# Kernel tuning notes

Hardware: AMD Instinct MI355X
Metric: run time of the kernel (lower is better)

Reference implementation:

```python
import jax, jax.numpy as jnp
import numpy as np

N_USER = 100_000
N_ITEM = 50_000
N = N_USER + N_ITEM           # total nodes
E = 4_800_000                 # nnz of normalized adjacency (avg degree 32)
D = 64                        # embed_size
L = 3                         # number of propagation layers (layer_size=[64,64,64])
B = 4096                      # query batch
EPS = 1e-12                   # F.normalize eps


def setup_inputs() -> dict:
    key = jax.random.key(0)
    ks = jax.random.split(key, 11)
    return {
        "user_emb": jax.random.normal(ks[0], (N_USER, D), jnp.float32) * 0.1,
        "item_emb": jax.random.normal(ks[1], (N_ITEM, D), jnp.float32) * 0.1,
        "W_gc": jax.random.normal(ks[2], (L, D, D), jnp.float32) * 0.1,
        "b_gc": jax.random.normal(ks[3], (L, D), jnp.float32) * 0.01,
        "W_bi": jax.random.normal(ks[4], (L, D, D), jnp.float32) * 0.1,
        "b_bi": jax.random.normal(ks[5], (L, D), jnp.float32) * 0.01,
        # normalized adjacency values ~ 1/deg scale
        "adj_val": jax.random.uniform(ks[6], (E,), jnp.float32) * (1.0 / 32.0),
        "adj_row": jax.random.randint(ks[7], (E,), 0, N, dtype=jnp.int32),
        "adj_col": jax.random.randint(ks[8], (E,), 0, N, dtype=jnp.int32),
        "users": jax.random.randint(ks[9], (B,), 0, N_USER, dtype=jnp.int32),
        "items": jax.random.randint(ks[10], (B,), 0, N_ITEM, dtype=jnp.int32),
    }


def _l2_normalize(x):
    # matches torch.nn.functional.normalize(p=2, dim=1, eps=1e-12)
    n = jnp.sqrt(jnp.sum(x * x, axis=1, keepdims=True))
    return x / jnp.maximum(n, EPS)


def reference(user_emb, item_emb, W_gc, b_gc, W_bi, b_bi,
              adj_val, adj_row, adj_col, users, items):
    ego = jnp.concatenate([user_emb, item_emb], axis=0)   # [N, D]
    all_embeddings = [ego]
    for k in range(L):
        # sparse A_hat @ ego: gather neighbor rows, scale, scatter-add
        msgs = adj_val[:, None] * ego[adj_col]            # [E, D]
        side = jax.ops.segment_sum(msgs, adj_row, num_segments=N)  # [N, D]
        sum_emb = side @ W_gc[k] + b_gc[k]                # GCN branch
        bi_emb = (ego * side) @ W_bi[k] + b_bi[k]         # bi-interaction branch
        ego = jax.nn.leaky_relu(sum_emb + bi_emb, negative_slope=0.2)
        all_embeddings.append(_l2_normalize(ego))
    all_embeddings = jnp.concatenate(all_embeddings, axis=1)  # [N, (L+1)*D]
    u_g = all_embeddings[users]                                # [B, 256]
    i_g = all_embeddings[N_USER + items]                       # [B, 256]
    return u_g, i_g
```

## Files before the change

### kernel.cpp

```cpp
#include <hip/hip_runtime.h>
#include <hip/hip_bf16.h>


#define N_USER 100000
#define N_ITEM 50000
#define N_NODES 150000
#define NE 4800000
#define D 64
#define BROWS 128
#define NBUCK ((N_NODES + BROWS - 1) / BROWS)
#define BCAP 4480
#define NG (N_NODES / 16)
#define NCB 5
#define NBIN (BROWS * NCB)
#define GMW ((N_NODES + 31) / 32)
#define NGL (8192 / 16)

#define SUPSH 12
#define NSUP 37
#define SCAP 133120
#define STG1 (NSUP * SCAP)
#define CH1 4688
#define B1 ((NE + CH1 - 1) / CH1)
#define CPS 27
#define CH2 4931
#define B2 (NSUP * CPS)

typedef __hip_bfloat16 bf16;
typedef unsigned short u16;
typedef unsigned int u32;
typedef __attribute__((ext_vector_type(8))) short short8;
typedef __attribute__((ext_vector_type(4))) float float4v;

__device__ __forceinline__ float bits2f(u16 u) {
  return __uint_as_float(((unsigned int)u) << 16);
}
__device__ __forceinline__ u16 f2bits(float x) {
  union { bf16 h; u16 u; } c;
  c.h = __float2bfloat16(x);
  return c.u;
}
__device__ __forceinline__ float loadF(const void* p, long i, int f32) {
  if (f32) return ((const float*)p)[i];
  return bits2f(((const u16*)p)[i]);
}

__global__ void k_zero(int* __restrict__ p, int n) {
  int i = blockIdx.x * blockDim.x + threadIdx.x;
  if (i < n) p[i] = 0;
}

__global__ void k_detect(const u16* __restrict__ ue, int* __restrict__ flag) {
  int bad = 0;
  for (int t = threadIdx.x; t < 512; t += 256) {
    float f = fabsf(bits2f(ue[t]));
    if (!(f < 1e4f)) bad = 1;
  }
  if (bad) atomicOr(flag, 1);
}

__global__ void __launch_bounds__(1024) k_mark(const int* __restrict__ users,
                                               const int* __restrict__ items,
                                               u32* __restrict__ gmap,
                                               int* __restrict__ rowlist) {
  int tid = threadIdx.x;
  for (int i = tid; i < GMW; i += 1024) gmap[i] = 0;
  __syncthreads();
  for (int b = tid; b < 8192; b += 1024) {
    int r = (b < 4096) ? users[b] : (N_USER + items[b - 4096]);
    rowlist[b] = r;
    atomicOr(&gmap[r >> 5], 1u << (r & 31));
  }
}

__global__ void k_prepw(const void* __restrict__ Wgc, const void* __restrict__ bgc,
                        const void* __restrict__ Wbi, const void* __restrict__ bbi,
                        u16* __restrict__ wfrag, float* __restrict__ biasws,
                        const int* __restrict__ flag) {
  int f32 = *flag;
  int layer = blockIdx.x;
  for (int f = threadIdx.x; f < 8192; f += 512) {
    int j = f & 7;
    int lane = (f >> 3) & 63;
    int s2 = (f >> 9) & 3;
    int t = f >> 11;
    int k = s2 * 32 + (lane >> 4) * 8 + j;
    int n = t * 16 + (lane & 15);
    float w = (k < 64) ? loadF(Wgc, (long)layer * 4096 + k * 64 + n, f32)
                       : loadF(Wbi, (long)layer * 4096 + (k - 64) * 64 + n, f32);
    wfrag[layer * 8192 + f] = f2bits(w);
  }
  if (threadIdx.x < 64)
    biasws[layer * 64 + threadIdx.x] =
        loadF(bgc, layer * 64 + threadIdx.x, f32) +
        loadF(bbi, layer * 64 + threadIdx.x, f32);
}

__global__ void k_init(const void* __restrict__ ue, const void* __restrict__ ie,
                       float* __restrict__ ego32, u16* __restrict__ egobf,
                       const int* __restrict__ flag, const u32* __restrict__ gmap) {
  int f32 = *flag;
  int i4 = (blockIdx.x * blockDim.x + threadIdx.x) * 4;
  if (i4 >= N_NODES * D) return;
  const int UD = N_USER * D;
  float4 v;
  ushort4 b;
  if (f32) {
    const float* s = (i4 < UD) ? ((const float*)ue + i4) : ((const float*)ie + (i4 - UD));
    v = *(const float4*)s;
    b = make_ushort4(f2bits(v.x), f2bits(v.y), f2bits(v.z), f2bits(v.w));
  } else {
    const u16* s = (i4 < UD) ? ((const u16*)ue + i4) : ((const u16*)ie + (i4 - UD));
    b = *(const ushort4*)s;
    v = make_float4(bits2f(b.x), bits2f(b.y), bits2f(b.z), bits2f(b.w));
  }
  int r = i4 >> 6;
  if ((gmap[r >> 5] >> (r & 31)) & 1) *(float4*)(ego32 + i4) = v;
  *(ushort4*)(egobf + i4) = b;
}

__global__ void __launch_bounds__(512, 8) k_bin1(
    const int* __restrict__ row, const int* __restrict__ col,
    const void* __restrict__ val, int* __restrict__ scnt,
    int2* __restrict__ staged1, const int* __restrict__ flag) {
  __shared__ int2 sbuf[CH1];
  __shared__ int hist[NSUP];
  __shared__ int lstart[NSUP];
  __shared__ int gbase[NSUP];
  __shared__ int lcur[NSUP];
  int f32 = *flag;
  int tid = threadIdx.x;
  int e0 = blockIdx.x * CH1;
  int e1 = min(e0 + CH1, NE);
  if (tid < NSUP) hist[tid] = 0;
  __syncthreads();
  for (int e = e0 + tid * 4; e < e1; e += 512 * 4) {
    int4 r4 = *(const int4*)(row + e);
    atomicAdd(&hist[r4.x >> SUPSH], 1);
    atomicAdd(&hist[r4.y >> SUPSH], 1);
    atomicAdd(&hist[r4.z >> SUPSH], 1);
    atomicAdd(&hist[r4.w >> SUPSH], 1);
  }
  __syncthreads();
  int resv = 0;
  if (tid < 64) {
    int h = (tid < NSUP) ? hist[tid] : 0;
    int inc = h;
#pragma unroll
    for (int off = 1; off < 64; off <<= 1) {
      int v = __shfl_up(inc, off);
      if (tid >= off) inc += v;
    }
    if (tid < NSUP) {
      int ex = inc - h;
      lstart[tid] = ex;
      lcur[tid] = ex;
      if (h) resv = atomicAdd(&scnt[tid], h);
    }
  }
  __syncthreads();
  for (int e = e0 + tid * 4; e < e1; e += 512 * 4) {
    int4 r4 = *(const int4*)(row + e);
    int4 c4 = *(const int4*)(col + e);
    int vb[4];
    if (f32) {
      float4 v4 = *(const float4*)((const float*)val + e);
      vb[0] = __float_as_int(v4.x); vb[1] = __float_as_int(v4.y);
      vb[2] = __float_as_int(v4.z); vb[3] = __float_as_int(v4.w);
    } else {
      ushort4 v4 = *(const ushort4*)((const u16*)val + e);
      vb[0] = __float_as_int(bits2f(v4.x)); vb[1] = __float_as_int(bits2f(v4.y));
      vb[2] = __float_as_int(bits2f(v4.z)); vb[3] = __float_as_int(bits2f(v4.w));
    }
    int rr[4] = {r4.x, r4.y, r4.z, r4.w};
    int cc[4] = {c4.x, c4.y, c4.z, c4.w};
#pragma unroll
    for (int j = 0; j < 4; ++j) {
      int s = rr[j] >> SUPSH;
      int pos = atomicAdd(&lcur[s], 1);
      sbuf[pos] = make_int2(((rr[j] & 4095) << 18) | cc[j], vb[j]);
    }
  }
  if (tid < NSUP) gbase[tid] = resv;
  __syncthreads();
  int wv = tid >> 6;
  int ln = tid & 63;
  for (int s = wv; s < NSUP; s += 8) {
    int h = hist[s];
    int gb = gbase[s];
    int ls = lstart[s];
    if (gb + h > SCAP) h = max(0, SCAP - gb);
    int2* dst = staged1 + (size_t)s * SCAP + gb;
    for (int i = ln; i < h; i += 64) dst[i] = sbuf[ls + i];
  }
}

__global__ void __launch_bounds__(512, 8) k_bin2(
    const int* __restrict__ scnt, const int2* __restrict__ staged1,
    int* __restrict__ bcnt, int2* __restrict__ staged2) {
  __shared__ int2 sbuf[CH2];
  __shared__ int hist[32];
  __shared__ int lstart[32];
  __shared__ int gbase[32];
  __shared__ int lcur[32];
  int tid = threadIdx.x;
  int sup = blockIdx.x / CPS;
  int e0 = (blockIdx.x % CPS) * CH2;
  int n = min(scnt[sup], SCAP);
  int e1 = min(e0 + CH2, n);
  if (e0 >= e1) return;
  const int2* seg = staged1 + (size_t)sup * SCAP;
  if (tid < 32) hist[tid] = 0;
  __syncthreads();
  {
    int e = e0 + tid * 2;
    for (; e + 1 < e1; e += 1024) {
      int4 two = *(const int4*)(seg + e);
      atomicAdd(&hist[two.x >> 25], 1);
      atomicAdd(&hist[two.z >> 25], 1);
    }
    if (e < e1) atomicAdd(&hist[seg[e].x >> 25], 1);
  }
  __syncthreads();
  int resv = 0;
  if (tid < 64) {
    int h = (tid < 32) ? hist[tid & 31] : 0;
    int inc = h;
#pragma unroll
    for (int off = 1; off < 32; off <<= 1) {
      int v = __shfl_up(inc, off);
      if (tid >= off) inc += v;
    }
    if (tid < 32) {
      int ex = inc - h;
      lstart[tid] = ex;
      lcur[tid] = ex;
      if (h) resv = atomicAdd(&bcnt[sup * 32 + tid], h);
    }
  }
  __syncthreads();
  {
    int e = e0 + tid * 2;
    for (; e + 1 < e1; e += 1024) {
      int4 two = *(const int4*)(seg + e);
      int lb0 = two.x >> 25;
      int p0 = atomicAdd(&lcur[lb0], 1);
      sbuf[p0] = make_int2(two.x & 0x01FFFFFF, two.y);
      int lb1 = two.z >> 25;
      int p1 = atomicAdd(&lcur[lb1], 1);
      sbuf[p1] = make_int2(two.z & 0x01FFFFFF, two.w);
    }
    if (e < e1) {
      int2 ent = seg[e];
      int lb = ent.x >> 25;
      int pos = atomicAdd(&lcur[lb], 1);
      sbuf[pos] = make_int2(ent.x & 0x01FFFFFF, ent.y);
    }
  }
  if (tid < 32) gbase[tid] = resv;
  __syncthreads();
  int wv = tid >> 6;
  int ln = tid & 63;
  for (int lb = wv; lb < 32; lb += 8) {
    int h = hist[lb];
    int gb = gbase[lb];
    int ls = lstart[lb];
    int b = sup * 32 + lb;
    if (b >= NBUCK) continue;
    if (gb + h > BCAP) h = max(0, BCAP - gb);
    int2* dst = staged2 + (size_t)b * BCAP + gb;
    for (int i = ln; i < h; i += 64) dst[i] = sbuf[ls + i];
  }
}

__global__ void __launch_bounds__(1024) k_bucketbase(const int* __restrict__ bcnt,
                                                     int* __restrict__ bbase) {
  __shared__ int sh[2048];
  int tid = threadIdx.x;
  int t0 = (tid < NBUCK) ? min(bcnt[tid], BCAP) : 0;
  int i1 = 1024 + tid;
  int t1 = (i1 < NBUCK) ? min(bcnt[i1], BCAP) : 0;
  sh[tid] = t0;
  sh[i1] = t1;
  __syncthreads();
  for (int off = 1; off < 2048; off <<= 1) {
    int a0 = (tid >= off) ? sh[tid - off] : 0;
    int a1 = (i1 >= off) ? sh[i1 - off] : 0;
    __syncthreads();
    sh[tid] += a0;
    sh[i1] += a1;
    __syncthreads();
  }
  if (tid < NBUCK) bbase[tid] = sh[tid] - t0;
  if (i1 < NBUCK) bbase[i1] = sh[i1] - t1;
}

__global__ void __launch_bounds__(512, 8) k_sortbucket(
    const int* __restrict__ bcnt, const int2* __restrict__ staged,
    const int* __restrict__ bbase, int* __restrict__ rp, int2* __restrict__ csr) {
  __shared__ int2 sbuf[BCAP];
  __shared__ int hist[NBIN];
  int tid = threadIdx.x;
  int b = blockIdx.x;
  for (int i = tid; i < NBIN; i += 512) hist[i] = 0;
  __syncthreads();

  int n = min(bcnt[b], BCAP);
  const int2* seg = staged + (size_t)b * BCAP;
  {
    int e = tid * 2;
    for (; e + 1 < n; e += 1024) {
      int4 two = *(const int4*)(seg + e);
      atomicAdd(&hist[(two.x >> 18) * NCB + ((two.x >> 15) & 7)], 1);
      atomicAdd(&hist[(two.z >> 18) * NCB + ((two.z >> 15) & 7)], 1);
    }
    if (e < n) {
      int x = seg[e].x;
      atomicAdd(&hist[(x >> 18) * NCB + ((x >> 15) & 7)], 1);
    }
  }
  __syncthreads();

  int i0 = tid, i1 = tid + 512;
  int h0 = hist[i0];
  int h1 = (i1 < NBIN) ? hist[i1] : 0;
  for (int off = 1; off < NBIN; off <<= 1) {
    int v0 = (i0 >= off) ? hist[i0 - off] : 0;
    int v1 = (i1 < NBIN && i1 >= off) ? hist[i1 - off] : 0;
    __syncthreads();
    hist[i0] += v0;
    if (i1 < NBIN) hist[i1] += v1;
    __syncthreads();
  }
  hist[i0] -= h0;
  if (i1 < NBIN) hist[i1] -= h1;
  __syncthreads();

  int base_b = bbase[b];
  if (tid < BROWS) {
    int r = b * BROWS + tid;
    if (r < N_NODES) rp[r] = base_b + hist[tid * NCB];
  }
  if (b == 0 && tid == 0) rp[N_NODES] = NE;
  __syncthreads();

  {
    int e = tid * 2;
    for (; e + 1 < n; e += 1024) {
      int4 two = *(const int4*)(seg + e);
      int k0 = (two.x >> 18) * NCB + ((two.x >> 15) & 7);
      int p0 = atomicAdd(&hist[k0], 1);
      if (p0 < BCAP) sbuf[p0] = make_int2(two.x & 0x3FFFF, two.y);
      int k1 = (two.z >> 18) * NCB + ((two.z >> 15) & 7);
      int p1 = atomicAdd(&hist[k1], 1);
      if (p1 < BCAP) sbuf[p1] = make_int2(two.z & 0x3FFFF, two.w);
    }
    if (e < n) {
      int2 ent = seg[e];
      int k = (ent.x >> 18) * NCB + ((ent.x >> 15) & 7);
      int pos = atomicAdd(&hist[k], 1);
      if (pos < BCAP) sbuf[pos] = make_int2(ent.x & 0x3FFFF, ent.y);
    }
  }
  __syncthreads();

  for (int i = tid; i < n; i += 512) csr[(size_t)base_b + i] = sbuf[i];
}

__global__ void __launch_bounds__(256, 8) k_layer(
    const int* __restrict__ rp, const int2* __restrict__ csr,
    const u16* __restrict__ egobf_i,
    const u16* __restrict__ wfrag, const float* __restrict__ biasws,
    float* __restrict__ ego32_o, u16* __restrict__ egobf_o, int layer,
    const u32* __restrict__ gmap, int last,
    const int* __restrict__ rowlist, int use_list) {
  __shared__ u16 tile[2176];
  int tid = threadIdx.x;
  int lane = tid & 63;
  int ln = lane & 15;
  int quad = lane >> 4;
  int wv = tid >> 6;
  int tg = blockIdx.x;
  const u16* wf = wfrag + layer * 8192;

  {
    int rid = tg * 16 + wv * 4 + quad;
    int r = use_list ? rowlist[rid] : rid;
    int s = rp[r];
    int e = rp[r + 1];
    float4 acc = make_float4(0.f, 0.f, 0.f, 0.f);
    int i = s;
    for (; i + 8 <= e; i += 8) {
      int2 cc[8];
#pragma unroll
      for (int t = 0; t < 8; ++t) cc[t] = csr[i + t];
      ushort4 gg[8];
#pragma unroll
      for (int t = 0; t < 8; ++t)
        gg[t] = *(const ushort4*)(egobf_i + (size_t)cc[t].x * 64 + ln * 4);
#pragma unroll
      for (int t = 0; t < 8; ++t) {
        float v = __int_as_float(cc[t].y);
        acc.x += v * bits2f(gg[t].x);
        acc.y += v * bits2f(gg[t].y);
        acc.z += v * bits2f(gg[t].z);
        acc.w += v * bits2f(gg[t].w);
      }
    }
    for (; i < e; ++i) {
      int2 c = csr[i];
      ushort4 g = *(const ushort4*)(egobf_i + (size_t)c.x * 64 + ln * 4);
      float v = __int_as_float(c.y);
      acc.x += v * bits2f(g.x);
      acc.y += v * bits2f(g.y);
      acc.z += v * bits2f(g.z);
      acc.w += v * bits2f(g.w);
    }
    ushort4 eb = *(const ushort4*)(egobf_i + (size_t)r * 64 + ln * 4);
    float4 er = make_float4(bits2f(eb.x), bits2f(eb.y), bits2f(eb.z), bits2f(eb.w));
    u16* trow = tile + (wv * 4 + quad) * 136;
    *(ushort4*)(trow + ln * 4) =
        make_ushort4(f2bits(acc.x), f2bits(acc.y), f2bits(acc.z), f2bits(acc.w));
    *(ushort4*)(trow + 64 + ln * 4) =
        make_ushort4(f2bits(er.x * acc.x), f2bits(er.y * acc.y),
                     f2bits(er.z * acc.z), f2bits(er.w * acc.w));
  }
  __syncthreads();

  float4v acc2 = (float4v){0.f, 0.f, 0.f, 0.f};
#pragma unroll
  for (int s2 = 0; s2 < 4; ++s2) {
    short8 A = *(const short8*)(tile + (size_t)ln * 136 + s2 * 32 + quad * 8);
    short8 Bf = *(const short8*)(wf + ((size_t)((wv * 4 + s2) * 64 + lane)) * 8);
    acc2 = __builtin_amdgcn_mfma_f32_16x16x32_bf16(A, Bf, acc2, 0, 0, 0);
  }
  int r0 = tg * 16;
  float bt = biasws[layer * 64 + wv * 16 + ln];
#pragma unroll
  for (int g2 = 0; g2 < 4; ++g2) {
    int rid2 = r0 + quad * 4 + g2;
    int rr = use_list ? rowlist[rid2] : rid2;
    float x = acc2[g2] + bt;
    x = fmaxf(x, 0.2f * x);
    size_t idx = (size_t)rr * 64 + wv * 16 + ln;
    if ((gmap[rr >> 5] >> (rr & 31)) & 1) ego32_o[idx] = x;
    if (!last) egobf_o[idx] = f2bits(x);
  }
}

__global__ void k_gather(const float* __restrict__ ego, const int* __restrict__ users,
                         const int* __restrict__ items, void* __restrict__ out,
                         int slice, int do_norm, const int* __restrict__ flag) {
  int f32 = *flag;
  int b = blockIdx.x * 4 + (threadIdx.x >> 6);
  int lane = threadIdx.x & 63;
  if (b >= 8192) return;
  int r = (b < 4096) ? users[b] : (N_USER + items[b - 4096]);
  float x = ego[(size_t)r * D + lane];
  float scale = 1.f;
  if (do_norm) {
    float ss = x * x;
    for (int off = 32; off > 0; off >>= 1) ss += __shfl_xor(ss, off);
    scale = 1.f / fmaxf(sqrtf(ss), 1e-12f);
  }
  float y = x * scale;
  long idx = (long)b * 256 + slice * 64 + lane;
  if (f32) ((float*)out)[idx] = y;
  else ((bf16*)out)[idx] = __float2bfloat16(y);
}

extern "C" void kernel_launch(void* const* d_in, const int* in_sizes, int n_in,
                              void* d_out, int out_size, void* d_ws, size_t ws_size,
                              hipStream_t stream) {
  const void* ue = d_in[0];
  const void* ie = d_in[1];
  const void* Wgc = d_in[2];
  const void* bgc = d_in[3];
  const void* Wbi = d_in[4];
  const void* bbi = d_in[5];
  const void* aval = d_in[6];
  const int* arow = (const int*)d_in[7];
  const int* acol = (const int*)d_in[8];
  const int* users = (const int*)d_in[9];
  const int* items = (const int*)d_in[10];

  char* ws = (char*)d_ws;
  size_t off = 0;
  float* ego32a = (float*)(ws + off); off += (size_t)N_NODES * D * 4;
  u16* egobfa = (u16*)(ws + off);     off += (size_t)N_NODES * D * 2;
  float* ego32b = (float*)(ws + off); off += (size_t)N_NODES * D * 4;
  u16* egobfb = (u16*)(ws + off);     off += (size_t)N_NODES * D * 2;
  int2* staged = (int2*)(ws + off);   off += (size_t)NBUCK * BCAP * 8;
  int2* csr = (int2*)(ws + off);      off += (size_t)STG1 * 8;
  int* rp = (int*)(ws + off);         off += (size_t)(N_NODES + 64) * 4;
  int* bcnt = (int*)(ws + off);       off += (size_t)NBUCK * 4;
  int* scnt = (int*)(ws + off);       off += 64 * 4;
  int* bbase = (int*)(ws + off);      off += (size_t)(NBUCK + 64) * 4;
  int* flag = (int*)(ws + off);       off += 256;
  u16* wfrag = (u16*)(ws + off);      off += 3 * 8192 * 2;
  float* biasws = (float*)(ws + off); off += 3 * 64 * 4;
  u32* gmap = (u32*)(ws + off);       off += (size_t)GMW * 4;
  int* rowlist = (int*)(ws + off);    off += 8192 * 4;
  int2* staged1 = csr;
  (void)ws_size;

  k_zero<<<1, 64, 0, stream>>>(flag, 1);
  k_detect<<<1, 256, 0, stream>>>((const u16*)ue, flag);
  k_zero<<<(NBUCK + 64 + 255) / 256, 256, 0, stream>>>(bcnt, NBUCK + 64);
  k_mark<<<1, 1024, 0, stream>>>(users, items, gmap, rowlist);
  k_prepw<<<3, 512, 0, stream>>>(Wgc, bgc, Wbi, bbi, wfrag, biasws, flag);
  k_init<<<(N_NODES * D / 4 + 255) / 256, 256, 0, stream>>>(ue, ie, ego32a, egobfa, flag, gmap);
  k_gather<<<2048, 256, 0, stream>>>(ego32a, users, items, d_out, 0, 0, flag);
  k_bin1<<<B1, 512, 0, stream>>>(arow, acol, aval, scnt, staged1, flag);
  k_bin2<<<B2, 512, 0, stream>>>(scnt, staged1, bcnt, staged);
  k_bucketbase<<<1, 1024, 0, stream>>>(bcnt, bbase);
  k_sortbucket<<<NBUCK, 512, 0, stream>>>(bcnt, staged, bbase, rp, csr);

  float* ei32 = ego32a; u16* eibf = egobfa;
  float* eo32 = ego32b; u16* eobf = egobfb;
  for (int k = 0; k < 3; ++k) {
    int lastl = (k == 2) ? 1 : 0;
    int grid = lastl ? NGL : NG;
    k_layer<<<grid, 256, 0, stream>>>(rp, csr, eibf, wfrag, biasws,
                                      eo32, eobf, k, gmap, lastl,
                                      rowlist, lastl);
    k_gather<<<2048, 256, 0, stream>>>(eo32, users, items, d_out, k + 1, 1, flag);
    float* t32 = ei32; ei32 = eo32; eo32 = t32;
    u16* tbf = eibf; eibf = eobf; eobf = tbf;
  }
}
```

Before: 446.5 us.

## Merge second binning pass and bucket scan into a per-bucket super-segment filter sort

Drops the k_bin2 and k_bucketbase kernels. Each bucket block now scans its whole super-bucket segment, keeps its own entries through ballot-based compaction into shared memory, and sorts them locally. The CSR is written with a fixed per-bucket stride, using separate row start and end arrays, so no global prefix scan over buckets is needed. This removes two launches and one staging round trip, but each super-segment is now read 32 times, once by every bucket block that shares it.

New measurement: 553.7 us. 1.24x slower.

```diff
diff --git a/kernel.cpp b/kernel.cpp
--- a/kernel.cpp
+++ b/kernel.cpp
@@ -22,13 +22,11 @@
 #define STG1 (NSUP * SCAP)
 #define CH1 4688
 #define B1 ((NE + CH1 - 1) / CH1)
-#define CPS 27
-#define CH2 4931
-#define B2 (NSUP * CPS)
 
 typedef __hip_bfloat16 bf16;
 typedef unsigned short u16;
 typedef unsigned int u32;
+typedef unsigned long long u64;
 typedef __attribute__((ext_vector_type(8))) short short8;
 typedef __attribute__((ext_vector_type(4))) float float4v;
 
@@ -195,129 +193,60 @@
   }
 }
 
-__global__ void __launch_bounds__(512, 8) k_bin2(
+__global__ void __launch_bounds__(512, 8) k_sortsuper(
     const int* __restrict__ scnt, const int2* __restrict__ staged1,
-    int* __restrict__ bcnt, int2* __restrict__ staged2) {
-  __shared__ int2 sbuf[CH2];
-  __shared__ int hist[32];
-  __shared__ int lstart[32];
-  __shared__ int gbase[32];
-  __shared__ int lcur[32];
-  int tid = threadIdx.x;
-  int sup = blockIdx.x / CPS;
-  int e0 = (blockIdx.x % CPS) * CH2;
-  int n = min(scnt[sup], SCAP);
-  int e1 = min(e0 + CH2, n);
-  if (e0 >= e1) return;
-  const int2* seg = staged1 + (size_t)sup * SCAP;
-  if (tid < 32) hist[tid] = 0;
-  __syncthreads();
-  {
-    int e = e0 + tid * 2;
-    for (; e + 1 < e1; e += 1024) {
-      int4 two = *(const int4*)(seg + e);
-      atomicAdd(&hist[two.x >> 25], 1);
-      atomicAdd(&hist[two.z >> 25], 1);
-    }
-    if (e < e1) atomicAdd(&hist[seg[e].x >> 25], 1);
-  }
-  __syncthreads();
-  int resv = 0;
-  if (tid < 64) {
-    int h = (tid < 32) ? hist[tid & 31] : 0;
-    int inc = h;
-#pragma unroll
-    for (int off = 1; off < 32; off <<= 1) {
-      int v = __shfl_up(inc, off);
-      if (tid >= off) inc += v;
-    }
-    if (tid < 32) {
-      int ex = inc - h;
-      lstart[tid] = ex;
-      lcur[tid] = ex;
-      if (h) resv = atomicAdd(&bcnt[sup * 32 + tid], h);
-    }
-  }
-  __syncthreads();
-  {
-    int e = e0 + tid * 2;
-    for (; e + 1 < e1; e += 1024) {
-      int4 two = *(const int4*)(seg + e);
-      int lb0 = two.x >> 25;
-      int p0 = atomicAdd(&lcur[lb0], 1);
-      sbuf[p0] = make_int2(two.x & 0x01FFFFFF, two.y);
-      int lb1 = two.z >> 25;
-      int p1 = atomicAdd(&lcur[lb1], 1);
-      sbuf[p1] = make_int2(two.z & 0x01FFFFFF, two.w);
-    }
-    if (e < e1) {
-      int2 ent = seg[e];
-      int lb = ent.x >> 25;
-      int pos = atomicAdd(&lcur[lb], 1);
-      sbuf[pos] = make_int2(ent.x & 0x01FFFFFF, ent.y);
-    }
-  }
-  if (tid < 32) gbase[tid] = resv;
-  __syncthreads();
-  int wv = tid >> 6;
-  int ln = tid & 63;
-  for (int lb = wv; lb < 32; lb += 8) {
-    int h = hist[lb];
-    int gb = gbase[lb];
-    int ls = lstart[lb];
-    int b = sup * 32 + lb;
-    if (b >= NBUCK) continue;
-    if (gb + h > BCAP) h = max(0, BCAP - gb);
-    int2* dst = staged2 + (size_t)b * BCAP + gb;
-    for (int i = ln; i < h; i += 64) dst[i] = sbuf[ls + i];
-  }
-}
-
-__global__ void __launch_bounds__(1024) k_bucketbase(const int* __restrict__ bcnt,
-                                                     int* __restrict__ bbase) {
-  __shared__ int sh[2048];
-  int tid = threadIdx.x;
-  int t0 = (tid < NBUCK) ? min(bcnt[tid], BCAP) : 0;
-  int i1 = 1024 + tid;
-  int t1 = (i1 < NBUCK) ? min(bcnt[i1], BCAP) : 0;
-  sh[tid] = t0;
-  sh[i1] = t1;
-  __syncthreads();
-  for (int off = 1; off < 2048; off <<= 1) {
-    int a0 = (tid >= off) ? sh[tid - off] : 0;
-    int a1 = (i1 >= off) ? sh[i1 - off] : 0;
-    __syncthreads();
-    sh[tid] += a0;
-    sh[i1] += a1;
-    __syncthreads();
-  }
-  if (tid < NBUCK) bbase[tid] = sh[tid] - t0;
-  if (i1 < NBUCK) bbase[i1] = sh[i1] - t1;
-}
-
-__global__ void __launch_bounds__(512, 8) k_sortbucket(
-    const int* __restrict__ bcnt, const int2* __restrict__ staged,
-    const int* __restrict__ bbase, int* __restrict__ rp, int2* __restrict__ csr) {
+    int* __restrict__ rps, int* __restrict__ rpe, int2* __restrict__ csr) {
   __shared__ int2 sbuf[BCAP];
   __shared__ int hist[NBIN];
+  __shared__ int cnt;
   int tid = threadIdx.x;
   int b = blockIdx.x;
+  int sup = b >> 5;
+  int lb = b & 31;
   for (int i = tid; i < NBIN; i += 512) hist[i] = 0;
-  __syncthreads();
-
-  int n = min(bcnt[b], BCAP);
-  const int2* seg = staged + (size_t)b * BCAP;
-  {
-    int e = tid * 2;
-    for (; e + 1 < n; e += 1024) {
+  if (tid == 0) cnt = 0;
+  __syncthreads();
+
+  int n = min(scnt[sup], SCAP);
+  const int2* seg = staged1 + (size_t)sup * SCAP;
+  int lane = tid & 63;
+  u64 ltm = ((u64)1 << lane) - 1;
+  int iters = (n + 1023) >> 10;
+  for (int it = 0; it < iters; ++it) {
+    int e = (it << 10) + tid * 2;
+    int2 ent0, ent1;
+    bool m0 = false, m1 = false;
+    if (e + 1 < n) {
       int4 two = *(const int4*)(seg + e);
-      atomicAdd(&hist[(two.x >> 18) * NCB + ((two.x >> 15) & 7)], 1);
-      atomicAdd(&hist[(two.z >> 18) * NCB + ((two.z >> 15) & 7)], 1);
-    }
-    if (e < n) {
-      int x = seg[e].x;
-      atomicAdd(&hist[(x >> 18) * NCB + ((x >> 15) & 7)], 1);
-    }
+      ent0 = make_int2(two.x, two.y);
+      ent1 = make_int2(two.z, two.w);
+      m0 = ((two.x >> 25) == lb);
+      m1 = ((two.z >> 25) == lb);
+    } else if (e < n) {
+      ent0 = seg[e];
+      m0 = ((ent0.x >> 25) == lb);
+    }
+    u64 mask0 = __ballot(m0);
+    u64 mask1 = __ballot(m1);
+    int tot = __popcll(mask0) + __popcll(mask1);
+    int base = 0;
+    if (lane == 0 && tot) base = atomicAdd(&cnt, tot);
+    base = __shfl(base, 0);
+    if (m0) {
+      int off = base + __popcll(mask0 & ltm);
+      if (off < BCAP) sbuf[off] = ent0;
+    }
+    if (m1) {
+      int off = base + __popcll(mask0) + __popcll(mask1 & ltm);
+      if (off < BCAP) sbuf[off] = ent1;
+    }
+  }
+  __syncthreads();
+  int nn = min(cnt, BCAP);
+
+  for (int i = tid; i < nn; i += 512) {
+    int x = sbuf[i].x;
+    atomicAdd(&hist[((x >> 18) & 127) * NCB + ((x >> 15) & 7)], 1);
   }
   __syncthreads();
 
@@ -332,44 +261,30 @@
     if (i1 < NBIN) hist[i1] += v1;
     __syncthreads();
   }
+  int cbase = b * BCAP;
+  if (tid < BROWS) {
+    int r = b * BROWS + tid;
+    if (r < N_NODES) {
+      rps[r] = cbase + (tid ? hist[tid * NCB - 1] : 0);
+      rpe[r] = cbase + hist[tid * NCB + NCB - 1];
+    }
+  }
+  __syncthreads();
   hist[i0] -= h0;
   if (i1 < NBIN) hist[i1] -= h1;
   __syncthreads();
 
-  int base_b = bbase[b];
-  if (tid < BROWS) {
-    int r = b * BROWS + tid;
-    if (r < N_NODES) rp[r] = base_b + hist[tid * NCB];
-  }
-  if (b == 0 && tid == 0) rp[N_NODES] = NE;
-  __syncthreads();
-
-  {
-    int e = tid * 2;
-    for (; e + 1 < n; e += 1024) {
-      int4 two = *(const int4*)(seg + e);
-      int k0 = (two.x >> 18) * NCB + ((two.x >> 15) & 7);
-      int p0 = atomicAdd(&hist[k0], 1);
-      if (p0 < BCAP) sbuf[p0] = make_int2(two.x & 0x3FFFF, two.y);
-      int k1 = (two.z >> 18) * NCB + ((two.z >> 15) & 7);
-      int p1 = atomicAdd(&hist[k1], 1);
-      if (p1 < BCAP) sbuf[p1] = make_int2(two.z & 0x3FFFF, two.w);
-    }
-    if (e < n) {
-      int2 ent = seg[e];
-      int k = (ent.x >> 18) * NCB + ((ent.x >> 15) & 7);
-      int pos = atomicAdd(&hist[k], 1);
-      if (pos < BCAP) sbuf[pos] = make_int2(ent.x & 0x3FFFF, ent.y);
-    }
-  }
-  __syncthreads();
-
-  for (int i = tid; i < n; i += 512) csr[(size_t)base_b + i] = sbuf[i];
+  for (int i = tid; i < nn; i += 512) {
+    int2 ent = sbuf[i];
+    int k = ((ent.x >> 18) & 127) * NCB + ((ent.x >> 15) & 7);
+    int pos = atomicAdd(&hist[k], 1);
+    if (pos < BCAP) csr[(size_t)cbase + pos] = make_int2(ent.x & 0x3FFFF, ent.y);
+  }
 }
 
 __global__ void __launch_bounds__(256, 8) k_layer(
-    const int* __restrict__ rp, const int2* __restrict__ csr,
-    const u16* __restrict__ egobf_i,
+    const int* __restrict__ rps, const int* __restrict__ rpe,
+    const int2* __restrict__ csr, const u16* __restrict__ egobf_i,
     const u16* __restrict__ wfrag, const float* __restrict__ biasws,
     float* __restrict__ ego32_o, u16* __restrict__ egobf_o, int layer,
     const u32* __restrict__ gmap, int last,
@@ -386,8 +301,8 @@
   {
     int rid = tg * 16 + wv * 4 + quad;
     int r = use_list ? rowlist[rid] : rid;
-    int s = rp[r];
-    int e = rp[r + 1];
+    int s = rps[r];
+    int e = rpe[r];
     float4 acc = make_float4(0.f, 0.f, 0.f, 0.f);
     int i = s;
     for (; i + 8 <= e; i += 8) {
@@ -490,38 +405,34 @@
   u16* egobfa = (u16*)(ws + off);     off += (size_t)N_NODES * D * 2;
   float* ego32b = (float*)(ws + off); off += (size_t)N_NODES * D * 4;
   u16* egobfb = (u16*)(ws + off);     off += (size_t)N_NODES * D * 2;
-  int2* staged = (int2*)(ws + off);   off += (size_t)NBUCK * BCAP * 8;
-  int2* csr = (int2*)(ws + off);      off += (size_t)STG1 * 8;
-  int* rp = (int*)(ws + off);         off += (size_t)(N_NODES + 64) * 4;
-  int* bcnt = (int*)(ws + off);       off += (size_t)NBUCK * 4;
+  int2* csr = (int2*)(ws + off);      off += (size_t)NBUCK * BCAP * 8;
+  int2* staged1 = (int2*)(ws + off);  off += (size_t)STG1 * 8;
+  int* rps = (int*)(ws + off);        off += (size_t)(N_NODES + 64) * 4;
+  int* rpe = (int*)(ws + off);        off += (size_t)(N_NODES + 64) * 4;
   int* scnt = (int*)(ws + off);       off += 64 * 4;
-  int* bbase = (int*)(ws + off);      off += (size_t)(NBUCK + 64) * 4;
   int* flag = (int*)(ws + off);       off += 256;
   u16* wfrag = (u16*)(ws + off);      off += 3 * 8192 * 2;
   float* biasws = (float*)(ws + off); off += 3 * 64 * 4;
   u32* gmap = (u32*)(ws + off);       off += (size_t)GMW * 4;
   int* rowlist = (int*)(ws + off);    off += 8192 * 4;
-  int2* staged1 = csr;
   (void)ws_size;
 
   k_zero<<<1, 64, 0, stream>>>(flag, 1);
   k_detect<<<1, 256, 0, stream>>>((const u16*)ue, flag);
-  k_zero<<<(NBUCK + 64 + 255) / 256, 256, 0, stream>>>(bcnt, NBUCK + 64);
+  k_zero<<<1, 64, 0, stream>>>(scnt, 64);
   k_mark<<<1, 1024, 0, stream>>>(users, items, gmap, rowlist);
   k_prepw<<<3, 512, 0, stream>>>(Wgc, bgc, Wbi, bbi, wfrag, biasws, flag);
   k_init<<<(N_NODES * D / 4 + 255) / 256, 256, 0, stream>>>(ue, ie, ego32a, egobfa, flag, gmap);
   k_gather<<<2048, 256, 0, stream>>>(ego32a, users, items, d_out, 0, 0, flag);
   k_bin1<<<B1, 512, 0, stream>>>(arow, acol, aval, scnt, staged1, flag);
-  k_bin2<<<B2, 512, 0, stream>>>(scnt, staged1, bcnt, staged);
-  k_bucketbase<<<1, 1024, 0, stream>>>(bcnt, bbase);
-  k_sortbucket<<<NBUCK, 512, 0, stream>>>(bcnt, staged, bbase, rp, csr);
+  k_sortsuper<<<NBUCK, 512, 0, stream>>>(scnt, staged1, rps, rpe, csr);
 
   float* ei32 = ego32a; u16* eibf = egobfa;
   float* eo32 = ego32b; u16* eobf = egobfb;
   for (int k = 0; k < 3; ++k) {
     int lastl = (k == 2) ? 1 : 0;
     int grid = lastl ? NGL : NG;
-    k_layer<<<grid, 256, 0, stream>>>(rp, csr, eibf, wfrag, biasws,
+    k_layer<<<grid, 256, 0, stream>>>(rps, rpe, csr, eibf, wfrag, biasws,
                                       eo32, eobf, k, gmap, lastl,
                                       rowlist, lastl);
     k_gather<<<2048, 256, 0, stream>>>(eo32, users, items, d_out, k + 1, 1, flag);
```
